# Optimization experiments

Measured on AMD Instinct MI355X. Metric: run time of the kernel, lower is better.

The kernel has to match this reference:

```python
import jax, jax.numpy as jnp
import numpy as np

K = 16        # max_points
S = 3         # num_scales
D_MODEL = 256
KDIM = 16
TAU = 1e-4
B_BATCH = 512


def _boundaries(k):
    edges = [(i, j) for i in range(k) for j in range(i + 1, k)]
    tris = [(i, j, kk) for i in range(k) for j in range(i + 1, k) for kk in range(j + 1, k)]
    E, T = len(edges), len(tris)
    B1 = np.zeros((k, E), np.float32)
    for e, (i, j) in enumerate(edges):
        B1[i, e] = -1.0
        B1[j, e] = 1.0
    e2i = {e: idx for idx, e in enumerate(edges)}
    B2 = np.zeros((E, T), np.float32)
    for t, (i, j, kk) in enumerate(tris):
        B2[e2i[(j, kk)], t] = 1.0
        B2[e2i[(i, kk)], t] = -1.0
        B2[e2i[(i, j)], t] = 1.0
    e_i = np.array([e[0] for e in edges], np.int32)
    e_j = np.array([e[1] for e in edges], np.int32)
    t_ij = np.array([e2i[(a, b)] for (a, b, c) in tris], np.int32)
    t_jk = np.array([e2i[(b, c)] for (a, b, c) in tris], np.int32)
    t_ik = np.array([e2i[(a, c)] for (a, b, c) in tris], np.int32)
    return B1, B2, e_i, e_j, t_ij, t_jk, t_ik


def setup_inputs() -> dict:
    key = jax.random.key(0)
    ks = jax.random.split(key, 8)
    d = D_MODEL
    B1, B2, e_i, e_j, t_ij, t_jk, t_ik = _boundaries(K)

    def lin(kk, fin, fout):
        return jax.random.normal(kk, (fin, fout), jnp.float32) / np.sqrt(fin).astype(np.float32)

    return dict(
        x=jax.random.normal(ks[0], (B_BATCH, K, d), jnp.float32),
        mask=jnp.ones((B_BATCH, K), jnp.float32),
        B1=jnp.asarray(B1), B2=jnp.asarray(B2), abs_B1=jnp.asarray(np.abs(B1)),
        e_i=jnp.asarray(e_i), e_j=jnp.asarray(e_j),
        t_ij=jnp.asarray(t_ij), t_jk=jnp.asarray(t_jk), t_ik=jnp.asarray(t_ik),
        log_scales=jnp.linspace(-1.5, 1.5, S).astype(jnp.float32),
        Wg=lin(ks[1], d, KDIM), bg=jnp.zeros((KDIM,), jnp.float32),
        Wv0=lin(ks[2], d, d * S), bv0=jnp.zeros((d * S,), jnp.float32),
        We=lin(ks[3], d, d * S), be=jnp.zeros((d * S,), jnp.float32),
        Wout=lin(ks[4], 2 * S * d, d), bout=jnp.zeros((d,), jnp.float32),
        g1=jnp.ones((d,), jnp.float32), b1=jnp.zeros((d,), jnp.float32),
        g2=jnp.ones((d,), jnp.float32), b2=jnp.zeros((d,), jnp.float32),
        Wf1=lin(ks[5], d, 4 * d), bf1=jnp.zeros((4 * d,), jnp.float32),
        Wf2=lin(ks[6], 4 * d, d), bf2=jnp.zeros((d,), jnp.float32),
    )


def _layernorm(x, g, b):
    mu = jnp.mean(x, -1, keepdims=True)
    var = jnp.mean(jnp.square(x - mu), -1, keepdims=True)
    return (x - mu) * jax.lax.rsqrt(var + 1e-5) * g + b


def _forward(x, mask, B1, B2, abs_B1, e_i, e_j, t_ij, t_jk, t_ik,
             log_scales, Wg, bg, Wv0, bv0, We, be, Wout, bout,
             g1, b1, g2, b2, Wf1, bf1, Wf2, bf2):
    B, Kp, d = x.shape
    E = B1.shape[1]
    residual = x
    x_norm = _layernorm(x, g1, b1)
    P = x_norm @ Wg + bg                                   # (B,K,k_dim)
    mask2 = mask[:, :, None] * mask[:, None, :]            # (B,K,K)
    # cdist (safe sqrt: zero diag, no NaN grads)
    pn = jnp.sum(P * P, -1)
    d2 = jnp.maximum(pn[:, :, None] + pn[:, None, :] - 2.0 * jnp.einsum('bik,bjk->bij', P, P), 0.0)
    Dm = jnp.where(d2 > 0, jnp.sqrt(jnp.where(d2 > 0, d2, 1.0)), 0.0) * mask2
    sigma_sq = jnp.square(jnp.exp(log_scales))             # (S,)
    A = jnp.exp(-(Dm * Dm)[:, None] / (2.0 * sigma_sq[None, :, None, None] + 1e-8)) * mask2[:, None]  # (B,S,K,K)
    W1 = A[:, :, e_i, e_j]                                 # (B,S,E) edge gather
    W2 = W1[:, :, t_ij] * W1[:, :, t_jk] * W1[:, :, t_ik]  # (B,S,T) triangle weights
    V0 = (x_norm @ Wv0 + bv0).reshape(B, Kp, S, d).transpose(0, 2, 1, 3)         # (B,S,K,d)
    E_raw = jnp.einsum('ke,bkd->bed', abs_B1, x_norm)                            # (B,E,d)
    E_in = (E_raw @ We + be).reshape(B, E, S, d).transpose(0, 2, 1, 3)           # (B,S,E,d)
    # L0 = B1 diag(W1) B1^T + tau I
    L0 = jnp.einsum('ke,bse,me->bskm', B1, W1, B1) + TAU * jnp.eye(Kp, dtype=x.dtype)
    M0 = jnp.einsum('bskm,bsmd->bskd', L0, V0)
    # L1 = B1^T diag(mask) B1 + B2 diag(W2) B2^T + tau I
    term_down = jnp.einsum('ke,bk,kf->bef', B1, mask, B1)                        # (B,E,E)
    term_up = jnp.einsum('et,bst,ft->bsef', B2, W2, B2)                          # (B,S,E,E)
    L1 = term_down[:, None] + term_up + TAU * jnp.eye(E, dtype=x.dtype)
    M1 = jnp.einsum('bsef,bsfd->bsed', L1, E_in)
    M1n = jnp.einsum('ke,bsed->bskd', abs_B1, M1)                                # edges -> nodes
    node_cat = M0.transpose(0, 2, 1, 3).reshape(B, Kp, S * d)
    edge_cat = M1n.transpose(0, 2, 1, 3).reshape(B, Kp, S * d)
    attn = jnp.concatenate([node_cat, edge_cat], -1) @ Wout + bout
    x2 = residual + attn                                   # dropout is identity in eval
    h = jax.nn.gelu(_layernorm(x2, g2, b2) @ Wf1 + bf1, approximate=False) @ Wf2 + bf2
    return x2 + h


def reference(x, mask, B1, B2, abs_B1, e_i, e_j, t_ij, t_jk, t_ik,
              log_scales, Wg, bg, Wv0, bv0, We, be, Wout, bout,
              g1, b1, g2, b2, Wf1, bf1, Wf2, bf2):
    return _forward(x, mask, B1, B2, abs_B1, e_i, e_j, t_ij, t_jk, t_ik,
                    log_scales, Wg, bg, Wv0, bv0, We, be, Wout, bout,
                    g1, b1, g2, b2, Wf1, bf1, Wf2, bf2)
```

## Files before the change

kernel.cpp:

```cpp
#include <hip/hip_runtime.h>
#include <math.h>

#define KN 16
#define DM 256
#define NS 3
#define NE 120
#define NT_TRI 560
#define NBATCH 512
#define TAUF 1e-4f
#define KAUG 1664

typedef unsigned short ushort_t;
typedef __attribute__((ext_vector_type(8))) short short8v;
typedef __attribute__((ext_vector_type(4))) short short4v;
typedef __attribute__((ext_vector_type(4))) float f32x4;

#define OFF_WSTACK 0u
#define OFF_WF1T   851968u
#define OFF_WF2T   1376256u
#define OFF_TOPO   1900544u
#define OFF_Z      1908736u
#define OFF_H      1908736u

__device__ __forceinline__ ushort_t f2bf(float f) {
    union { float f; unsigned int u; } v; v.f = f;
    unsigned int r = v.u + 0x7FFFu + ((v.u >> 16) & 1u);
    return (ushort_t)(r >> 16);
}
__device__ __forceinline__ void gload_lds16(const void* g, void* l) {
    auto gp = (const __attribute__((address_space(1))) unsigned int*)(unsigned long long)(g);
    auto lp = (__attribute__((address_space(3))) unsigned int*)(unsigned long long)(l);
    __builtin_amdgcn_global_load_lds(gp, lp, 16, 0, 0);
}

__global__ __launch_bounds__(256) void prep_kernel(
    const float* __restrict__ Wv0, const float* __restrict__ bv0,
    const float* __restrict__ We,  const float* __restrict__ be,
    const float* __restrict__ Wout,
    const float* __restrict__ Wf1, const float* __restrict__ Wf2,
    const int* __restrict__ e_i, const int* __restrict__ e_j,
    const int* __restrict__ t_ij, const int* __restrict__ t_jk, const int* __restrict__ t_ik,
    ushort_t* __restrict__ wstack, ushort_t* __restrict__ wf1t,
    ushort_t* __restrict__ wf2t,
    float* __restrict__ topoF, int* __restrict__ triPk)
{
    __shared__ float lhs[16][DM];
    __shared__ float tile[64][65];
    __shared__ int   eidxL[256];
    const int bid = blockIdx.x;
    const int j = threadIdx.x;

    if (bid == 230) {
        eidxL[j] = -1;
        __syncthreads();
        if (j < NE) {
            const int i = e_i[j], jn = e_j[j];
            eidxL[i*16 + jn] = j; eidxL[jn*16 + i] = j;
        }
        __syncthreads();
        const int n = j >> 4, m = j & 15;
        float q, p2, adj;
        if (n != m) {
            const int e = eidxL[j];
            if (e >= 0) { q = (m == e_j[e]) ? 1.f : -1.f; p2 = 1.f; adj = 1.f; }
            else        { q = 0.f; p2 = 0.f; adj = 0.f; }
        } else {
            q = 0.f; p2 = 0.f; adj = 0.f;
            for (int kk = 0; kk < KN; ++kk) {
                if (kk == n) continue;
                const int e = eidxL[n*16 + kk];
                if (e >= 0) { q += (n == e_j[e]) ? 1.f : -1.f; p2 += 1.f; }
            }
        }
        topoF[j] = q; topoF[256 + j] = p2; topoF[512 + j] = adj;
        for (int tt = j; tt < NT_TRI; tt += 256) {
            const int eij = t_ij[tt], ejk = t_jk[tt], eik = t_ik[tt];
            const int a0 = e_i[eij], a1 = e_j[eij];
            const int b0 = e_i[ejk], b1v = e_j[ejk];
            const int c0 = e_i[eik], c1 = e_j[eik];
            const int mid = (b0 == a0 || b0 == a1) ? b0 : b1v;
            triPk[2*tt]   = a0 | (a1 << 8) | (b0 << 16) | (b1v << 24);
            triPk[2*tt+1] = c0 | (c1 << 8) | (mid << 16);
        }
        return;
    }

    if (bid < 102) {
        const int m = bid / 17, by = bid % 17;
        const int path = m / 3, s = m % 3;
        const float* __restrict__ Wo = Wout + (size_t)m*DM*DM;
        if (by == 16) {
            const float* bv = (path == 0) ? bv0 : be;
            const float f = (path == 0) ? 1.0f : 0.5f;
            float acc = 0.f;
            for (int k = 0; k < DM; ++k)
                acc += bv[s*DM + k] * f * Wo[k*DM + j];
            wstack[(size_t)j*KAUG + 1536 + m] = f2bf(acc);
            if (m == 0)
                for (int c = 1542; c < KAUG; ++c)
                    wstack[(size_t)j*KAUG + c] = 0;
            return;
        }
        const float* src = (path == 0) ? Wv0 : We;
        const int i0 = by * 16;
        for (int r = 0; r < 16; ++r)
            lhs[r][j] = src[(size_t)(i0 + r)*(NS*DM) + s*DM + j];
        __syncthreads();
        float acc[16];
#pragma unroll
        for (int r = 0; r < 16; ++r) acc[r] = 0.f;
        for (int k = 0; k < DM; ++k) {
            const float w = Wo[k*DM + j];
#pragma unroll
            for (int r = 0; r < 16; ++r) acc[r] += lhs[r][k] * w;
        }
#pragma unroll
        for (int r = 0; r < 16; ++r)
            wstack[(size_t)j*KAUG + m*DM + i0 + r] = f2bf(acc[r]);
        return;
    }

    const float* in; ushort_t* outp; int R, C, rt, ct;
    if (bid < 166) {
        const int q = bid - 102;
        in = Wf1; outp = wf1t; R = 256; C = 1024;
        rt = (q >> 4) * 64; ct = (q & 15) * 64;
    } else {
        const int q = bid - 166;
        in = Wf2; outp = wf2t; R = 1024; C = 256;
        rt = (q >> 2) * 64; ct = (q & 3) * 64;
    }
#pragma unroll
    for (int q2 = 0; q2 < 16; ++q2) {
        const int idx = q2*256 + j;
        const int r = idx >> 6, c = idx & 63;
        tile[r][c] = in[(size_t)(rt + r)*C + ct + c];
    }
    __syncthreads();
#pragma unroll
    for (int q2 = 0; q2 < 16; ++q2) {
        const int idx = q2*256 + j;
        const int cc = idx >> 6, rr = idx & 63;
        outp[(size_t)(ct + cc)*R + rt + rr] = f2bf(tile[rr][cc]);
    }
}

__global__ __launch_bounds__(256) void attn_topo_kernel(
    const float* __restrict__ x, const float* __restrict__ mask,
    const float* __restrict__ log_scales,
    const float* __restrict__ Wg, const float* __restrict__ bg,
    const float* __restrict__ g1, const float* __restrict__ b1,
    const float* __restrict__ topoF, const int* __restrict__ triPk,
    ushort_t* __restrict__ Z)
{
    const int b = blockIdx.x;
    const int t = threadIdx.x;
    const int n = t >> 4, m = t & 15;

    __shared__ ushort_t xnbT[DM][32];
    __shared__ float Plds[KN][KN];
    __shared__ float mskL[KN];
    __shared__ float QL[256];
    __shared__ float P2L[256];
    __shared__ float adjL[256];
    __shared__ float sA[NS][KN][KN];
    __shared__ float Hupd[NS*KN];
    __shared__ ushort_t Tbf[6][KN][32];

    QL[t]  = topoF[t];
    P2L[t] = topoF[256 + t];
    adjL[t] = topoF[512 + t];
    if (t < KN) mskL[t] = mask[b*KN + t];
    {
        const short8v z8 = {0,0,0,0,0,0,0,0};
        *(short8v*)&xnbT[t][16] = z8;
        *(short8v*)&xnbT[t][24] = z8;
    }

    float xv[16];
    {
        const int cg = m * 16;
        const float* xr = x + (size_t)(b*KN + n)*DM + cg;
        const f32x4 v0 = *(const f32x4*)(xr);
        const f32x4 v1 = *(const f32x4*)(xr + 4);
        const f32x4 v2 = *(const f32x4*)(xr + 8);
        const f32x4 v3 = *(const f32x4*)(xr + 12);
#pragma unroll
        for (int q = 0; q < 4; ++q) { xv[q] = v0[q]; xv[4+q] = v1[q]; xv[8+q] = v2[q]; xv[12+q] = v3[q]; }
        float ssum = 0.f;
#pragma unroll
        for (int q = 0; q < 16; ++q) ssum += xv[q];
#pragma unroll
        for (int o = 1; o < 16; o <<= 1) ssum += __shfl_xor(ssum, o);
        const float mu = ssum * (1.f/DM);
        float vsum = 0.f;
#pragma unroll
        for (int q = 0; q < 16; ++q) { const float d = xv[q]-mu; vsum += d*d; }
#pragma unroll
        for (int o = 1; o < 16; o <<= 1) vsum += __shfl_xor(vsum, o);
        const float rstd = rsqrtf(vsum*(1.f/DM) + 1e-5f);
        const f32x4 ga = *(const f32x4*)(g1 + cg),   gb = *(const f32x4*)(g1 + cg + 4);
        const f32x4 gc = *(const f32x4*)(g1 + cg + 8), gd = *(const f32x4*)(g1 + cg + 12);
        const f32x4 ba = *(const f32x4*)(b1 + cg),   bb = *(const f32x4*)(b1 + cg + 4);
        const f32x4 bc = *(const f32x4*)(b1 + cg + 8), bd = *(const f32x4*)(b1 + cg + 12);
        float gg[16], bbv[16];
#pragma unroll
        for (int q = 0; q < 4; ++q) {
            gg[q] = ga[q]; gg[4+q] = gb[q]; gg[8+q] = gc[q]; gg[12+q] = gd[q];
            bbv[q] = ba[q]; bbv[4+q] = bb[q]; bbv[8+q] = bc[q]; bbv[12+q] = bd[q];
        }
#pragma unroll
        for (int q = 0; q < 16; ++q) {
            xv[q] = (xv[q]-mu)*rstd*gg[q] + bbv[q];
            xnbT[cg + q][n] = f2bf(xv[q]);
        }
    }

    {
        float part[16];
#pragma unroll
        for (int c = 0; c < 16; ++c) part[c] = 0.f;
        const int cg = m * 16;
#pragma unroll
        for (int q = 0; q < 16; ++q) {
            const float xq = xv[q];
            const float* wr = Wg + (size_t)(cg + q)*KN;
            const f32x4 w0 = *(const f32x4*)(wr);
            const f32x4 w1 = *(const f32x4*)(wr + 4);
            const f32x4 w2 = *(const f32x4*)(wr + 8);
            const f32x4 w3 = *(const f32x4*)(wr + 12);
            part[0]  += xq*w0[0]; part[1]  += xq*w0[1]; part[2]  += xq*w0[2]; part[3]  += xq*w0[3];
            part[4]  += xq*w1[0]; part[5]  += xq*w1[1]; part[6]  += xq*w1[2]; part[7]  += xq*w1[3];
            part[8]  += xq*w2[0]; part[9]  += xq*w2[1]; part[10] += xq*w2[2]; part[11] += xq*w2[3];
            part[12] += xq*w3[0]; part[13] += xq*w3[1]; part[14] += xq*w3[2]; part[15] += xq*w3[3];
        }
        const int b0 = t & 1, b1b = (t>>1)&1, b2 = (t>>2)&1, b3 = (t>>3)&1;
        float p8[8];
#pragma unroll
        for (int c2 = 0; c2 < 8; ++c2) {
            const float keep = b0 ? part[2*c2+1] : part[2*c2];
            const float send = b0 ? part[2*c2]   : part[2*c2+1];
            p8[c2] = keep + __shfl_xor(send, 1);
        }
        float p4[4];
#pragma unroll
        for (int c2 = 0; c2 < 4; ++c2) {
            const float keep = b1b ? p8[2*c2+1] : p8[2*c2];
            const float send = b1b ? p8[2*c2]   : p8[2*c2+1];
            p4[c2] = keep + __shfl_xor(send, 2);
        }
        float p2v[2];
#pragma unroll
        for (int c2 = 0; c2 < 2; ++c2) {
            const float keep = b2 ? p4[2*c2+1] : p4[2*c2];
            const float send = b2 ? p4[2*c2]   : p4[2*c2+1];
            p2v[c2] = keep + __shfl_xor(send, 4);
        }
        const float keep = b3 ? p2v[1] : p2v[0];
        const float send = b3 ? p2v[0] : p2v[1];
        Plds[n][m] = keep + __shfl_xor(send, 8) + bg[m];
    }
    __syncthreads();

    float T0[NS], hq;
    {
        float d2 = 0.f;
#pragma unroll
        for (int k = 0; k < KN; ++k) {
            const float dd = Plds[n][k] - Plds[m][k];
            d2 += dd*dd;
        }
        const float m2v = mskL[n]*mskL[m];
        const float dm = (d2 > 0.f) ? sqrtf(d2)*m2v : 0.f;
        const float dmsq = dm*dm;
        const float adjv = adjL[t];
#pragma unroll
        for (int s = 0; s < NS; ++s) {
            const float sig2 = expf(2.f*log_scales[s]);
            const float a = expf(-dmsq/(2.f*sig2 + 1e-8f)) * m2v;
            sA[s][n][m] = a;
            const float am = a * adjv;
            float rsum = am;
#pragma unroll
            for (int o = 1; o < 16; o <<= 1) rsum += __shfl_xor(rsum, o);
            const float tv = (m == n) ? (TAUF + rsum) : (-am);
            T0[s] = tv;
            Tbf[s][n][m] = f2bf(tv);
        }
        hq = 0.f;
#pragma unroll
        for (int k = 0; k < KN; ++k)
            hq += mskL[k]*QL[n*16 + k]*QL[m*16 + k];
        if (t < NS*KN) Hupd[t] = 0.f;
#pragma unroll
        for (int idx = 0; idx < 6; ++idx) {
            const int e2 = idx*256 + t;
            Tbf[e2 >> 8][(e2 >> 4) & 15][16 + (e2 & 15)] = 0;
        }
    }
    __syncthreads();

    for (int tt = t; tt < NT_TRI; tt += 256) {
        const int w0 = triPk[2*tt], w1 = triPk[2*tt+1];
        const int a0 = w0 & 255, a1 = (w0 >> 8) & 255;
        const int b0 = (w0 >> 16) & 255, b1v = (w0 >> 24) & 255;
        const int c0 = w1 & 255, c1 = (w1 >> 8) & 255, mid = (w1 >> 16) & 255;
#pragma unroll
        for (int s = 0; s < NS; ++s)
            atomicAdd(&Hupd[s*KN + mid],
                      4.f * sA[s][a0][a1] * sA[s][b0][b1v] * sA[s][c0][c1]);
    }
    __syncthreads();

    ushort_t* Zb = Z + (size_t)b*KN*KAUG;
    {
        float T1[NS];
        const float p2v = P2L[t];
#pragma unroll
        for (int s = 0; s < NS; ++s) {
            const float tv = hq + TAUF*p2v + ((m == n) ? Hupd[s*KN + n] : 0.f);
            T1[s] = tv;
            Tbf[NS + s][n][m] = f2bf(tv);
        }
        float sv[6] = {T0[0], T0[1], T0[2], T1[0], T1[1], T1[2]};
#pragma unroll
        for (int q = 0; q < 6; ++q) {
            float v = sv[q];
#pragma unroll
            for (int o = 1; o < 16; o <<= 1) v += __shfl_xor(v, o);
            sv[q] = v;
        }
        const float wv = (m==0)?sv[0]:(m==1)?sv[1]:(m==2)?sv[2]:(m==3)?sv[3]:(m==4)?sv[4]:sv[5];
        if (m < 6) Zb[(size_t)n*KAUG + 1536 + m] = f2bf(wv);
        for (int idx = t; idx < 122*KN; idx += 256) {
            const int nn = idx / 122, c = 1542 + idx % 122;
            Zb[(size_t)nn*KAUG + c] = 0;
        }
    }
    __syncthreads();

    {
        const int w = t >> 6, l = t & 63;
        const int lr = l & 15, lk = l >> 4;
        short8v bfrT[6];
#pragma unroll
        for (int m6 = 0; m6 < 6; ++m6)
            bfrT[m6] = *(const short8v*)&Tbf[m6][lr][lk*8];
#pragma unroll
        for (int q4 = 0; q4 < 4; ++q4) {
            const int jb = w*64 + q4*16;
            const short8v axn = *(const short8v*)&xnbT[jb + lr][lk*8];
#pragma unroll
            for (int m6 = 0; m6 < 6; ++m6) {
                f32x4 acc = {0.f,0.f,0.f,0.f};
                acc = __builtin_amdgcn_mfma_f32_16x16x32_bf16(axn, bfrT[m6], acc, 0, 0, 0);
                short4v zv;
#pragma unroll
                for (int rg = 0; rg < 4; ++rg) zv[rg] = (short)f2bf(acc[rg]);
                *(short4v*)(Zb + (size_t)lr*KAUG + m6*256 + jb + lk*4) = zv;
            }
        }
    }
}

template<int BM, int BN, int BK, int KD, int EPI>
__global__ __launch_bounds__(256) void gemm_lds(
    const ushort_t* __restrict__ A, const ushort_t* __restrict__ Bt,
    const float* __restrict__ bias, const float* __restrict__ resid,
    float* __restrict__ outF, ushort_t* __restrict__ outH, int ldo)
{
    constexpr int ROWB = BK*2;
    constexpr int KS = BK/32;
    constexpr int MF = BM/32, NF = BN/32;
    constexpr int APASS = BM*ROWB/4096;
    constexpr int BPASS = BN*ROWB/4096;
    __shared__ ushort_t lA[BM*BK];
    __shared__ ushort_t lB[BN*BK];
    const int t = threadIdx.x;
    const int w = t >> 6, l = t & 63;
    const int wm = w & 1, wn = w >> 1;
    const int lr = l & 15, lk = l >> 4;
    const int brow = blockIdx.x * BM;
    const int bcol = blockIdx.y * BN;

    f32x4 acc[MF][NF];
#pragma unroll
    for (int mf = 0; mf < MF; ++mf)
#pragma unroll
        for (int nt = 0; nt < NF; ++nt)
            acc[mf][nt] = (f32x4){0.f,0.f,0.f,0.f};

    const int byteoff = t * 16;

    for (int kc = 0; kc < KD/BK; ++kc) {
        if (kc) __syncthreads();
#pragma unroll
        for (int c = 0; c < APASS; ++c) {
            const int bo = c*4096 + byteoff;
            const int row = bo / ROWB;
            const int gs = ((bo % ROWB) >> 4) ^ (row & 7);
            gload_lds16(A + (size_t)(brow + row)*KD + kc*BK + gs*8, lA + (bo >> 1));
        }
#pragma unroll
        for (int c = 0; c < BPASS; ++c) {
            const int bo = c*4096 + byteoff;
            const int row = bo / ROWB;
            const int gs = ((bo % ROWB) >> 4) ^ (row & 7);
            gload_lds16(Bt + (size_t)(bcol + row)*KD + kc*BK + gs*8, lB + (bo >> 1));
        }
        __syncthreads();
#pragma unroll
        for (int ks = 0; ks < KS; ++ks) {
            short8v af[MF], bfr[NF];
#pragma unroll
            for (int mf = 0; mf < MF; ++mf) {
                const int ra = wm*(BM/2) + mf*16 + lr;
                const int gs = (ks*4 + lk) ^ (ra & 7);
                af[mf] = *(const short8v*)(lA + ra*BK + gs*8);
            }
#pragma unroll
            for (int nt = 0; nt < NF; ++nt) {
                const int rb = wn*(BN/2) + nt*16 + lr;
                const int gs = (ks*4 + lk) ^ (rb & 7);
                bfr[nt] = *(const short8v*)(lB + rb*BK + gs*8);
            }
#pragma unroll
            for (int mf = 0; mf < MF; ++mf)
#pragma unroll
                for (int nt = 0; nt < NF; ++nt)
                    acc[mf][nt] = __builtin_amdgcn_mfma_f32_16x16x32_bf16(
                        af[mf], bfr[nt], acc[mf][nt], 0, 0, 0);
        }
    }

#pragma unroll
    for (int mf = 0; mf < MF; ++mf) {
#pragma unroll
        for (int nt = 0; nt < NF; ++nt) {
            const int col = bcol + wn*(BN/2) + nt*16 + lr;
#pragma unroll
            for (int rg = 0; rg < 4; ++rg) {
                const int row = brow + wm*(BM/2) + mf*16 + lk*4 + rg;
                const size_t o = (size_t)row * ldo + col;
                const float v = acc[mf][nt][rg];
                if (EPI == 2) {
                    outF[o] = outF[o] + v + bias[col];
                } else {
                    outF[o] = resid[o] + v + bias[col];
                }
            }
        }
    }
}

__global__ __launch_bounds__(256) void gemm_ffn1(
    const float* __restrict__ x2, const float* __restrict__ gv,
    const float* __restrict__ bv,
    const ushort_t* __restrict__ Bt, const float* __restrict__ bias,
    ushort_t* __restrict__ outH)
{
    constexpr int BM = 64, BN = 128, KD = 256, BK = 64, ROWB = BK*2;
    __shared__ ushort_t lnA[BM*KD];
    __shared__ ushort_t lB[BN*BK];
    const int t = threadIdx.x;
    const int w = t >> 6, l = t & 63;
    const int wm = w & 1, wn = w >> 1;
    const int lr = l & 15, lk = l >> 4;
    const int brow = blockIdx.x * BM;
    const int bcol = blockIdx.y * BN;

    {
        const int row = t >> 2, c0 = (t & 3) * 64;
        const float* xr = x2 + (size_t)(brow + row)*DM + c0;
        f32x4 va[16];
        float s = 0.f;
#pragma unroll
        for (int q = 0; q < 16; ++q) {
            va[q] = *(const f32x4*)(xr + q*4);
            s += va[q][0] + va[q][1] + va[q][2] + va[q][3];
        }
        s += __shfl_xor(s, 1); s += __shfl_xor(s, 2);
        const float mu = s * (1.f/DM);
        float vs = 0.f;
#pragma unroll
        for (int q = 0; q < 16; ++q) {
#pragma unroll
            for (int i = 0; i < 4; ++i) { const float d = va[q][i]-mu; vs += d*d; }
        }
        vs += __shfl_xor(vs, 1); vs += __shfl_xor(vs, 2);
        const float rstd = rsqrtf(vs*(1.f/DM) + 1e-5f);
#pragma unroll
        for (int q = 0; q < 16; q += 2) {
            short8v o;
#pragma unroll
            for (int i = 0; i < 4; ++i) {
                const int c = c0 + q*4 + i;
                o[i] = (short)f2bf((va[q][i]-mu)*rstd*gv[c] + bv[c]);
            }
#pragma unroll
            for (int i = 0; i < 4; ++i) {
                const int c = c0 + (q+1)*4 + i;
                o[4+i] = (short)f2bf((va[q+1][i]-mu)*rstd*gv[c] + bv[c]);
            }
            const int g = (c0 >> 3) + (q >> 1);
            const int gs = g ^ (row & 7);
            *(short8v*)(lnA + row*KD + gs*8) = o;
        }
    }

    f32x4 acc[2][4];
#pragma unroll
    for (int mf = 0; mf < 2; ++mf)
#pragma unroll
        for (int nt = 0; nt < 4; ++nt)
            acc[mf][nt] = (f32x4){0.f,0.f,0.f,0.f};

    const int byteoff = t * 16;
    for (int kc = 0; kc < KD/BK; ++kc) {
        __syncthreads();
#pragma unroll
        for (int c = 0; c < 4; ++c) {
            const int bo = c*4096 + byteoff;
            const int row = bo / ROWB;
            const int gs = ((bo % ROWB) >> 4) ^ (row & 7);
            gload_lds16(Bt + (size_t)(bcol + row)*KD + kc*BK + gs*8, lB + (bo >> 1));
        }
        __syncthreads();
#pragma unroll
        for (int ks = 0; ks < 2; ++ks) {
            short8v af[2], bfr[4];
#pragma unroll
            for (int mf = 0; mf < 2; ++mf) {
                const int ra = wm*32 + mf*16 + lr;
                const int g = kc*8 + ks*4 + lk;
                const int gs = g ^ (ra & 7);
                af[mf] = *(const short8v*)(lnA + ra*KD + gs*8);
            }
#pragma unroll
            for (int nt = 0; nt < 4; ++nt) {
                const int rb = wn*64 + nt*16 + lr;
                const int gs = (ks*4 + lk) ^ (rb & 7);
                bfr[nt] = *(const short8v*)(lB + rb*BK + gs*8);
            }
#pragma unroll
            for (int mf = 0; mf < 2; ++mf)
#pragma unroll
                for (int nt = 0; nt < 4; ++nt)
                    acc[mf][nt] = __builtin_amdgcn_mfma_f32_16x16x32_bf16(
                        af[mf], bfr[nt], acc[mf][nt], 0, 0, 0);
        }
    }

#pragma unroll
    for (int mf = 0; mf < 2; ++mf) {
#pragma unroll
        for (int nt = 0; nt < 4; ++nt) {
            const int col = bcol + wn*64 + nt*16 + lr;
#pragma unroll
            for (int rg = 0; rg < 4; ++rg) {
                const int row = brow + wm*32 + mf*16 + lk*4 + rg;
                const float u = acc[mf][nt][rg] + bias[col];
                const float a = 0.79788456080286536f*(u + 0.044715f*u*u*u);
                outH[(size_t)row*1024 + col] = f2bf(u / (1.f + __expf(-2.f*a)));
            }
        }
    }
}

extern "C" void kernel_launch(void* const* d_in, const int* in_sizes, int n_in,
                              void* d_out, int out_size, void* d_ws, size_t ws_size,
                              hipStream_t stream) {
    const float* x          = (const float*)d_in[0];
    const float* mask       = (const float*)d_in[1];
    const int*   e_i        = (const int*)  d_in[5];
    const int*   e_j        = (const int*)  d_in[6];
    const int*   t_ij       = (const int*)  d_in[7];
    const int*   t_jk       = (const int*)  d_in[8];
    const int*   t_ik       = (const int*)  d_in[9];
    const float* log_scales = (const float*)d_in[10];
    const float* Wg         = (const float*)d_in[11];
    const float* bg         = (const float*)d_in[12];
    const float* Wv0        = (const float*)d_in[13];
    const float* bv0        = (const float*)d_in[14];
    const float* We         = (const float*)d_in[15];
    const float* be         = (const float*)d_in[16];
    const float* Wout       = (const float*)d_in[17];
    const float* bout       = (const float*)d_in[18];
    const float* g1         = (const float*)d_in[19];
    const float* b1         = (const float*)d_in[20];
    const float* g2         = (const float*)d_in[21];
    const float* b2         = (const float*)d_in[22];
    const float* Wf1        = (const float*)d_in[23];
    const float* bf1        = (const float*)d_in[24];
    const float* Wf2        = (const float*)d_in[25];
    const float* bf2        = (const float*)d_in[26];

    char* wsb = (char*)d_ws;
    ushort_t* wstack = (ushort_t*)(wsb + OFF_WSTACK);
    ushort_t* wf1t   = (ushort_t*)(wsb + OFF_WF1T);
    ushort_t* wf2t   = (ushort_t*)(wsb + OFF_WF2T);
    float*    topoF  = (float*)   (wsb + OFF_TOPO);
    int*      triPk  = (int*)     (wsb + OFF_TOPO + 3072);
    ushort_t* Z      = (ushort_t*)(wsb + OFF_Z);
    ushort_t* H      = (ushort_t*)(wsb + OFF_H);
    float*    out    = (float*)d_out;

    hipLaunchKernelGGL(prep_kernel, dim3(231), dim3(256), 0, stream,
                       Wv0, bv0, We, be, Wout, Wf1, Wf2,
                       e_i, e_j, t_ij, t_jk, t_ik,
                       wstack, wf1t, wf2t, topoF, triPk);
    hipLaunchKernelGGL(attn_topo_kernel, dim3(NBATCH), dim3(256), 0, stream,
                       x, mask, log_scales, Wg, bg, g1, b1, topoF, triPk, Z);
    hipLaunchKernelGGL((gemm_lds<64,64,128,KAUG,3>), dim3(128,4), dim3(256), 0, stream,
                       Z, wstack, bout, x, out, (ushort_t*)nullptr, 256);
    hipLaunchKernelGGL(gemm_ffn1, dim3(128,8), dim3(256), 0, stream,
                       out, g2, b2, wf1t, bf1, H);
    hipLaunchKernelGGL((gemm_lds<64,64,128,1024,2>), dim3(128,4), dim3(256), 0, stream,
                       H, wf2t, bf2, (const float*)nullptr,
                       out, (ushort_t*)nullptr, 256);
}
```

Baseline: 123.5 us.

## Split topology kernel, bucket triangles by middle vertex to replace LDS atomics

Triangles are pre-sorted by their middle vertex in the prep kernel, so the per-batch triangle accumulation becomes a plain per-(scale, vertex) reduction instead of shared-memory atomicAdds. The attention kernel is split in two: one computes the topology matrices and writes bf16 T and normalized-x tiles to workspace, and a second kernel reloads them through global-to-LDS loads and does the MFMA expansion into Z. It also switches to fast __expf. The split adds an extra launch and a global round trip of intermediates, and the sorted-triangle loop is serial per bucket.

```diff
diff --git a/kernel.cpp b/kernel.cpp
--- a/kernel.cpp
+++ b/kernel.cpp
@@ -19,8 +19,11 @@
 #define OFF_WF1T   851968u
 #define OFF_WF2T   1376256u
 #define OFF_TOPO   1900544u
-#define OFF_Z      1908736u
-#define OFF_H      1908736u
+#define OFF_RST    1908736u
+#define OFF_TBF    2105344u
+#define OFF_XNT    5251072u
+#define OFF_Z      13639680u
+#define OFF_H      13639680u
 
 __device__ __forceinline__ ushort_t f2bf(float f) {
     union { float f; unsigned int u; } v; v.f = f;
@@ -42,11 +45,12 @@
     const int* __restrict__ t_ij, const int* __restrict__ t_jk, const int* __restrict__ t_ik,
     ushort_t* __restrict__ wstack, ushort_t* __restrict__ wf1t,
     ushort_t* __restrict__ wf2t,
-    float* __restrict__ topoF, int* __restrict__ triPk)
+    float* __restrict__ topoF, int* __restrict__ midOff, int* __restrict__ triSrt)
 {
     __shared__ float lhs[16][DM];
     __shared__ float tile[64][65];
     __shared__ int   eidxL[256];
+    __shared__ int   cnts[16], offs[17];
     const int bid = blockIdx.x;
     const int j = threadIdx.x;
 
@@ -73,14 +77,39 @@
             }
         }
         topoF[j] = q; topoF[256 + j] = p2; topoF[512 + j] = adj;
-        for (int tt = j; tt < NT_TRI; tt += 256) {
-            const int eij = t_ij[tt], ejk = t_jk[tt], eik = t_ik[tt];
-            const int a0 = e_i[eij], a1 = e_j[eij];
-            const int b0 = e_i[ejk], b1v = e_j[ejk];
-            const int c0 = e_i[eik], c1 = e_j[eik];
-            const int mid = (b0 == a0 || b0 == a1) ? b0 : b1v;
-            triPk[2*tt]   = a0 | (a1 << 8) | (b0 << 16) | (b1v << 24);
-            triPk[2*tt+1] = c0 | (c1 << 8) | (mid << 16);
+
+        if (j < 16) {
+            int c = 0;
+            for (int tt = 0; tt < NT_TRI; ++tt) {
+                const int eij = t_ij[tt], ejk = t_jk[tt];
+                const int a0 = e_i[eij], a1 = e_j[eij];
+                const int b0 = e_i[ejk];
+                const int mid = (b0 == a0 || b0 == a1) ? b0 : e_j[ejk];
+                if (mid == j) ++c;
+            }
+            cnts[j] = c;
+        }
+        __syncthreads();
+        if (j == 0) {
+            int s = 0;
+            for (int q2 = 0; q2 < 16; ++q2) { offs[q2] = s; s += cnts[q2]; }
+            offs[16] = s;
+        }
+        __syncthreads();
+        if (j < 17) midOff[j] = offs[j];
+        if (j < 16) {
+            int w = offs[j];
+            for (int tt = 0; tt < NT_TRI; ++tt) {
+                const int eij = t_ij[tt], ejk = t_jk[tt], eik = t_ik[tt];
+                const int a0 = e_i[eij], a1 = e_j[eij];
+                const int b0 = e_i[ejk], b1v = e_j[ejk];
+                const int c0 = e_i[eik], c1 = e_j[eik];
+                const int mid = (b0 == a0 || b0 == a1) ? b0 : b1v;
+                if (mid == j) {
+                    const int ia = a0*16 + a1, ib = b0*16 + b1v, ic = c0*16 + c1;
+                    triSrt[w++] = ia | (ib << 8) | (ic << 16);
+                }
+            }
         }
         return;
     }
@@ -145,13 +174,15 @@
     }
 }
 
-__global__ __launch_bounds__(256) void attn_topo_kernel(
+__global__ __launch_bounds__(256) void topo_kernel(
     const float* __restrict__ x, const float* __restrict__ mask,
     const float* __restrict__ log_scales,
     const float* __restrict__ Wg, const float* __restrict__ bg,
     const float* __restrict__ g1, const float* __restrict__ b1,
-    const float* __restrict__ topoF, const int* __restrict__ triPk,
-    ushort_t* __restrict__ Z)
+    const float* __restrict__ topoF, const int* __restrict__ midOff,
+    const int* __restrict__ triSrt,
+    ushort_t* __restrict__ tbf, ushort_t* __restrict__ xnt,
+    float* __restrict__ rstOut)
 {
     const int b = blockIdx.x;
     const int t = threadIdx.x;
@@ -164,7 +195,7 @@
     __shared__ float P2L[256];
     __shared__ float adjL[256];
     __shared__ float sA[NS][KN][KN];
-    __shared__ float Hupd[NS*KN];
+    __shared__ float part[4][NS][KN];
     __shared__ ushort_t Tbf[6][KN][32];
 
     QL[t]  = topoF[t];
@@ -217,9 +248,9 @@
     }
 
     {
-        float part[16];
-#pragma unroll
-        for (int c = 0; c < 16; ++c) part[c] = 0.f;
+        float partc[16];
+#pragma unroll
+        for (int c = 0; c < 16; ++c) partc[c] = 0.f;
         const int cg = m * 16;
 #pragma unroll
         for (int q = 0; q < 16; ++q) {
@@ -229,17 +260,17 @@
             const f32x4 w1 = *(const f32x4*)(wr + 4);
             const f32x4 w2 = *(const f32x4*)(wr + 8);
             const f32x4 w3 = *(const f32x4*)(wr + 12);
-            part[0]  += xq*w0[0]; part[1]  += xq*w0[1]; part[2]  += xq*w0[2]; part[3]  += xq*w0[3];
-            part[4]  += xq*w1[0]; part[5]  += xq*w1[1]; part[6]  += xq*w1[2]; part[7]  += xq*w1[3];
-            part[8]  += xq*w2[0]; part[9]  += xq*w2[1]; part[10] += xq*w2[2]; part[11] += xq*w2[3];
-            part[12] += xq*w3[0]; part[13] += xq*w3[1]; part[14] += xq*w3[2]; part[15] += xq*w3[3];
+            partc[0]  += xq*w0[0]; partc[1]  += xq*w0[1]; partc[2]  += xq*w0[2]; partc[3]  += xq*w0[3];
+            partc[4]  += xq*w1[0]; partc[5]  += xq*w1[1]; partc[6]  += xq*w1[2]; partc[7]  += xq*w1[3];
+            partc[8]  += xq*w2[0]; partc[9]  += xq*w2[1]; partc[10] += xq*w2[2]; partc[11] += xq*w2[3];
+            partc[12] += xq*w3[0]; partc[13] += xq*w3[1]; partc[14] += xq*w3[2]; partc[15] += xq*w3[3];
         }
         const int b0 = t & 1, b1b = (t>>1)&1, b2 = (t>>2)&1, b3 = (t>>3)&1;
         float p8[8];
 #pragma unroll
         for (int c2 = 0; c2 < 8; ++c2) {
-            const float keep = b0 ? part[2*c2+1] : part[2*c2];
-            const float send = b0 ? part[2*c2]   : part[2*c2+1];
+            const float keep = b0 ? partc[2*c2+1] : partc[2*c2];
+            const float send = b0 ? partc[2*c2]   : partc[2*c2+1];
             p8[c2] = keep + __shfl_xor(send, 1);
         }
         float p4[4];
@@ -276,8 +307,8 @@
         const float adjv = adjL[t];
 #pragma unroll
         for (int s = 0; s < NS; ++s) {
-            const float sig2 = expf(2.f*log_scales[s]);
-            const float a = expf(-dmsq/(2.f*sig2 + 1e-8f)) * m2v;
+            const float sig2 = __expf(2.f*log_scales[s]);
+            const float a = __expf(-dmsq/(2.f*sig2 + 1e-8f)) * m2v;
             sA[s][n][m] = a;
             const float am = a * adjv;
             float rsum = am;
@@ -291,7 +322,6 @@
 #pragma unroll
         for (int k = 0; k < KN; ++k)
             hq += mskL[k]*QL[n*16 + k]*QL[m*16 + k];
-        if (t < NS*KN) Hupd[t] = 0.f;
 #pragma unroll
         for (int idx = 0; idx < 6; ++idx) {
             const int e2 = idx*256 + t;
@@ -300,25 +330,31 @@
     }
     __syncthreads();
 
-    for (int tt = t; tt < NT_TRI; tt += 256) {
-        const int w0 = triPk[2*tt], w1 = triPk[2*tt+1];
-        const int a0 = w0 & 255, a1 = (w0 >> 8) & 255;
-        const int b0 = (w0 >> 16) & 255, b1v = (w0 >> 24) & 255;
-        const int c0 = w1 & 255, c1 = (w1 >> 8) & 255, mid = (w1 >> 16) & 255;
-#pragma unroll
-        for (int s = 0; s < NS; ++s)
-            atomicAdd(&Hupd[s*KN + mid],
-                      4.f * sA[s][a0][a1] * sA[s][b0][b1v] * sA[s][c0][c1]);
+    {
+        const int c4 = t >> 6, rem = t & 63;
+        const int midb = rem & 15, sb = rem >> 4;
+        if (sb < NS) {
+            const float* sAf = &sA[sb][0][0];
+            float acc = 0.f;
+            const int lo = midOff[midb], hi = midOff[midb + 1];
+            for (int ii = lo + c4; ii < hi; ii += 4) {
+                const int pk = triSrt[ii];
+                acc += sAf[pk & 255] * sAf[(pk >> 8) & 255] * sAf[(pk >> 16) & 255];
+            }
+            part[c4][sb][midb] = 4.f * acc;
+        }
     }
     __syncthreads();
 
-    ushort_t* Zb = Z + (size_t)b*KN*KAUG;
     {
         float T1[NS];
         const float p2v = P2L[t];
 #pragma unroll
         for (int s = 0; s < NS; ++s) {
-            const float tv = hq + TAUF*p2v + ((m == n) ? Hupd[s*KN + n] : 0.f);
+            float hup = 0.f;
+            if (m == n)
+                hup = part[0][s][n] + part[1][s][n] + part[2][s][n] + part[3][s][n];
+            const float tv = hq + TAUF*p2v + hup;
             T1[s] = tv;
             Tbf[NS + s][n][m] = f2bf(tv);
         }
@@ -331,35 +367,71 @@
             sv[q] = v;
         }
         const float wv = (m==0)?sv[0]:(m==1)?sv[1]:(m==2)?sv[2]:(m==3)?sv[3]:(m==4)?sv[4]:sv[5];
-        if (m < 6) Zb[(size_t)n*KAUG + 1536 + m] = f2bf(wv);
-        for (int idx = t; idx < 122*KN; idx += 256) {
-            const int nn = idx / 122, c = 1542 + idx % 122;
-            Zb[(size_t)nn*KAUG + c] = 0;
-        }
+        if (m < 6) rstOut[(size_t)b*96 + m*16 + n] = wv;
     }
     __syncthreads();
 
     {
-        const int w = t >> 6, l = t & 63;
-        const int lr = l & 15, lk = l >> 4;
-        short8v bfrT[6];
-#pragma unroll
-        for (int m6 = 0; m6 < 6; ++m6)
-            bfrT[m6] = *(const short8v*)&Tbf[m6][lr][lk*8];
-#pragma unroll
-        for (int q4 = 0; q4 < 4; ++q4) {
-            const int jb = w*64 + q4*16;
-            const short8v axn = *(const short8v*)&xnbT[jb + lr][lk*8];
-#pragma unroll
-            for (int m6 = 0; m6 < 6; ++m6) {
-                f32x4 acc = {0.f,0.f,0.f,0.f};
-                acc = __builtin_amdgcn_mfma_f32_16x16x32_bf16(axn, bfrT[m6], acc, 0, 0, 0);
-                short4v zv;
-#pragma unroll
-                for (int rg = 0; rg < 4; ++rg) zv[rg] = (short)f2bf(acc[rg]);
-                *(short4v*)(Zb + (size_t)lr*KAUG + m6*256 + jb + lk*4) = zv;
-            }
-        }
+        const short8v* st = (const short8v*)&Tbf[0][0][0];
+        short8v* dt = (short8v*)(tbf + (size_t)b*3072);
+        dt[t] = st[t];
+        if (t < 128) dt[256 + t] = st[256 + t];
+        const short8v* sx = (const short8v*)&xnbT[0][0];
+        short8v* dx = (short8v*)(xnt + (size_t)b*8192);
+#pragma unroll
+        for (int q = 0; q < 4; ++q) dx[q*256 + t] = sx[q*256 + t];
+    }
+}
+
+__global__ __launch_bounds__(256) void zmfma_kernel(
+    const ushort_t* __restrict__ tbf, const ushort_t* __restrict__ xnt,
+    const float* __restrict__ rst, ushort_t* __restrict__ Z)
+{
+    const int b = blockIdx.x, t = threadIdx.x;
+    __shared__ ushort_t xnbT[DM][32];
+    __shared__ ushort_t Tbf[6][KN][32];
+    __shared__ float rs[96];
+
+    const ushort_t* xs = xnt + (size_t)b*8192;
+    const ushort_t* ts = tbf + (size_t)b*3072;
+#pragma unroll
+    for (int q = 0; q < 4; ++q)
+        gload_lds16(xs + (size_t)(q*256 + t)*8, ((ushort_t*)xnbT) + (q*256 + t)*8);
+    gload_lds16(ts + (size_t)t*8, ((ushort_t*)Tbf) + t*8);
+    if (t < 128)
+        gload_lds16(ts + (size_t)(256 + t)*8, ((ushort_t*)Tbf) + (256 + t)*8);
+    if (t < 96) rs[t] = rst[(size_t)b*96 + t];
+    __syncthreads();
+
+    ushort_t* Zb = Z + (size_t)b*KN*KAUG;
+    const int w = t >> 6, l = t & 63;
+    const int lr = l & 15, lk = l >> 4;
+    short8v bfrT[6];
+#pragma unroll
+    for (int m6 = 0; m6 < 6; ++m6)
+        bfrT[m6] = *(const short8v*)&Tbf[m6][lr][lk*8];
+#pragma unroll
+    for (int q4 = 0; q4 < 4; ++q4) {
+        const int jb = w*64 + q4*16;
+        const short8v axn = *(const short8v*)&xnbT[jb + lr][lk*8];
+#pragma unroll
+        for (int m6 = 0; m6 < 6; ++m6) {
+            f32x4 acc = {0.f,0.f,0.f,0.f};
+            acc = __builtin_amdgcn_mfma_f32_16x16x32_bf16(axn, bfrT[m6], acc, 0, 0, 0);
+            short4v zv;
+#pragma unroll
+            for (int rg = 0; rg < 4; ++rg) zv[rg] = (short)f2bf(acc[rg]);
+            *(short4v*)(Zb + (size_t)lr*KAUG + m6*256 + jb + lk*4) = zv;
+        }
+    }
+    {
+        const int row = t >> 4, grp = t & 15;
+        short8v tv = {0,0,0,0,0,0,0,0};
+        if (grp == 0) {
+#pragma unroll
+            for (int i = 0; i < 6; ++i) tv[i] = (short)f2bf(rs[i*16 + row]);
+        }
+        *(short8v*)(Zb + (size_t)row*KAUG + 1536 + grp*8) = tv;
     }
 }
 
@@ -600,7 +672,11 @@
     ushort_t* wf1t   = (ushort_t*)(wsb + OFF_WF1T);
     ushort_t* wf2t   = (ushort_t*)(wsb + OFF_WF2T);
     float*    topoF  = (float*)   (wsb + OFF_TOPO);
-    int*      triPk  = (int*)     (wsb + OFF_TOPO + 3072);
+    int*      midOff = (int*)     (wsb + OFF_TOPO + 3072);
+    int*      triSrt = (int*)     (wsb + OFF_TOPO + 3200);
+    float*    rst    = (float*)   (wsb + OFF_RST);
+    ushort_t* tbf    = (ushort_t*)(wsb + OFF_TBF);
+    ushort_t* xnt    = (ushort_t*)(wsb + OFF_XNT);
     ushort_t* Z      = (ushort_t*)(wsb + OFF_Z);
     ushort_t* H      = (ushort_t*)(wsb + OFF_H);
     float*    out    = (float*)d_out;
@@ -608,9 +684,12 @@
     hipLaunchKernelGGL(prep_kernel, dim3(231), dim3(256), 0, stream,
                        Wv0, bv0, We, be, Wout, Wf1, Wf2,
                        e_i, e_j, t_ij, t_jk, t_ik,
-                       wstack, wf1t, wf2t, topoF, triPk);
-    hipLaunchKernelGGL(attn_topo_kernel, dim3(NBATCH), dim3(256), 0, stream,
-                       x, mask, log_scales, Wg, bg, g1, b1, topoF, triPk, Z);
+                       wstack, wf1t, wf2t, topoF, midOff, triSrt);
+    hipLaunchKernelGGL(topo_kernel, dim3(NBATCH), dim3(256), 0, stream,
+                       x, mask, log_scales, Wg, bg, g1, b1,
+                       topoF, midOff, triSrt, tbf, xnt, rst);
+    hipLaunchKernelGGL(zmfma_kernel, dim3(NBATCH), dim3(256), 0, stream,
+                       tbf, xnt, rst, Z);
     hipLaunchKernelGGL((gemm_lds<64,64,128,KAUG,3>), dim3(128,4), dim3(256), 0, stream,
                        Z, wstack, bout, x, out, (ushort_t*)nullptr, 256);
     hipLaunchKernelGGL(gemm_ffn1, dim3(128,8), dim3(256), 0, stream,
```

Measured after the change: 291.5 us. 136% more time.
